# Performance work log

Measured on AMD Instinct MI355X. Metric: run time of the kernel, lower is better.

Reference implementation:

```python
import jax, jax.numpy as jnp
import numpy as np

B = 2097152  # batch of poses

def setup_inputs() -> dict:
    key = jax.random.key(0)
    ks = jax.random.split(key, 7)
    x = jax.random.normal(ks[0], (B, 7), dtype=jnp.float32)
    # PyTorch Linear init: U(-1/sqrt(fan_in), 1/sqrt(fan_in)); weights stored [out, in]
    def linear_params(kw, kb, fan_in, fan_out):
        bound = 1.0 / np.sqrt(fan_in)
        W = jax.random.uniform(kw, (fan_out, fan_in), minval=-bound, maxval=bound, dtype=jnp.float32)
        b = jax.random.uniform(kb, (fan_out,), minval=-bound, maxval=bound, dtype=jnp.float32)
        return W, b
    W1, b1 = linear_params(ks[1], ks[2], 7, 64)
    W2, b2 = linear_params(ks[3], ks[4], 64, 64)
    W3, b3 = linear_params(ks[5], ks[6], 64, 7)
    return {"x": x, "W1": W1, "b1": b1, "W2": W2, "b2": b2, "W3": W3, "b3": b3}

def reference(x, W1, b1, W2, b2, W3, b3):
    h = jax.nn.relu(x @ W1.T + b1)
    h = jax.nn.relu(h @ W2.T + b2)
    out = h @ W3.T + b3  # [B, 7]
    pos = out[:, :3]
    quat = out[:, 3:]
    quat = quat / jnp.linalg.norm(quat, axis=1, keepdims=True)
    return jnp.concatenate([pos, quat], axis=1)
```

## Files before the change

kernel.cpp:

```cpp
#include <hip/hip_runtime.h>
#include <math.h>


typedef _Float16 half8  __attribute__((ext_vector_type(8)));
typedef __fp16   fp16x2 __attribute__((ext_vector_type(2)));
typedef float    floatx16 __attribute__((ext_vector_type(16)));
typedef unsigned int uint2v __attribute__((ext_vector_type(2)));

#define MFMA32(a, b, c) __builtin_amdgcn_mfma_f32_32x32x16_f16((a), (b), (c), 0, 0, 0)
#define LO_SCALE 2.44140625e-4f

union PairU { fp16x2 h; unsigned int u; };
union FragU { unsigned int w[4]; half8 h; };

static __device__ inline void split_pack2(float v0, float v1,
                                          unsigned int& hw, unsigned int& lw) {
    PairU hp, lp;
    hp.h = __builtin_amdgcn_cvt_pkrtz(v0, v1);
    float f0 = (float)hp.h[0], f1 = (float)hp.h[1];
    lp.h = __builtin_amdgcn_cvt_pkrtz((v0 - f0) * 4096.0f,
                                      (v1 - f1) * 4096.0f);
    hw = hp.u; lw = lp.u;
}

static __device__ inline void swap32(unsigned int a, unsigned int b,
                                     unsigned int& lo, unsigned int& hi) {
    uint2v r = __builtin_amdgcn_permlane32_swap(a, b, false, false);
    lo = r[0]; hi = r[1];
}

__global__ __launch_bounds__(256, 2) void pose_mlp_mfma_t(
    const float* __restrict__ x,
    const float* __restrict__ W1, const float* __restrict__ b1,
    const float* __restrict__ W2, const float* __restrict__ b2,
    const float* __restrict__ W3, const float* __restrict__ b3,
    float* __restrict__ out, int nrows)
{
    const int tid  = threadIdx.x;
    const int lane = tid & 63;
    const int wv   = tid >> 6;
    const int g    = lane >> 5;
    const int n5   = lane & 31;

    half8 w2h[2][4], w2l[2][4];
#pragma unroll
    for (int ct = 0; ct < 2; ++ct) {
        const float* wrow = W2 + (ct * 32 + n5) * 64;
#pragma unroll
        for (int kb = 0; kb < 4; ++kb) {
            FragU H, L;
#pragma unroll
            for (int m = 0; m < 4; ++m) {
                float a0 = wrow[kb * 16 + g * 8 + 2 * m];
                float a1 = wrow[kb * 16 + g * 8 + 2 * m + 1];
                split_pack2(a0, a1, H.w[m], L.w[m]);
            }
            w2h[ct][kb] = H.h; w2l[ct][kb] = L.h;
        }
    }
    const bool nv = (n5 < 7);
    half8 w3h[4], w3l[4];
#pragma unroll
    for (int kb = 0; kb < 4; ++kb) {
        FragU H, L;
#pragma unroll
        for (int m = 0; m < 4; ++m) {
            float a0 = nv ? W3[n5 * 64 + kb * 16 + g * 8 + 2 * m] : 0.0f;
            float a1 = nv ? W3[n5 * 64 + kb * 16 + g * 8 + 2 * m + 1] : 0.0f;
            split_pack2(a0, a1, H.w[m], L.w[m]);
        }
        w3h[kb] = H.h; w3l[kb] = L.h;
    }
    half8 w1h[2], w1l[2];
#pragma unroll
    for (int ct = 0; ct < 2; ++ct) {
        FragU H, L;
#pragma unroll
        for (int m = 0; m < 4; ++m) {
            int k0 = 2 * m, k1 = 2 * m + 1;
            float a0 = (g == 0) ? W1[(ct * 32 + n5) * 7 + k0] : 0.0f;
            float a1 = (g == 0) ? ((k1 < 7) ? W1[(ct * 32 + n5) * 7 + k1]
                                            : b1[ct * 32 + n5]) : 0.0f;
            split_pack2(a0, a1, H.w[m], L.w[m]);
        }
        w1h[ct] = H.h; w1l[ct] = L.h;
    }
    float b2t[2][16];
#pragma unroll
    for (int ct = 0; ct < 2; ++ct)
#pragma unroll
        for (int i = 0; i < 16; ++i)
            b2t[ct][i] = b2[ct * 32 + (i & 3) + 8 * (i >> 2) + 4 * g];
    float b3t[4];
#pragma unroll
    for (int i = 0; i < 4; ++i)
        b3t[i] = g ? ((i < 3) ? b3[4 + i] : 0.0f) : b3[i];

    const int ITERS = 16;
    const int blk0 = blockIdx.x * (ITERS * 128);

    float xv[7] = {0.f,0.f,0.f,0.f,0.f,0.f,0.f};
    {
        int r = blk0 + wv * 32 + n5;
        if (g == 0 && r < nrows) {
            const float* xr = x + (size_t)r * 7;
#pragma unroll
            for (int j = 0; j < 7; ++j) xv[j] = xr[j];
        }
    }

    for (int it = 0; it < ITERS; ++it) {
        const int r0 = blk0 + it * 128 + wv * 32;

        FragU xH, xL;
        {
            float p0 = g ? 0.f : xv[0], p1 = g ? 0.f : xv[1];
            float p2 = g ? 0.f : xv[2], p3 = g ? 0.f : xv[3];
            float p4 = g ? 0.f : xv[4], p5 = g ? 0.f : xv[5];
            float p6 = g ? 0.f : xv[6], p7 = g ? 0.f : 1.0f;
            split_pack2(p0, p1, xH.w[0], xL.w[0]);
            split_pack2(p2, p3, xH.w[1], xL.w[1]);
            split_pack2(p4, p5, xH.w[2], xL.w[2]);
            split_pack2(p6, p7, xH.w[3], xL.w[3]);
        }
        if (it < ITERS - 1) {
            int r = r0 + 128 + n5;
            if (g == 0 && r < nrows) {
                const float* xr = x + (size_t)r * 7;
#pragma unroll
                for (int j = 0; j < 7; ++j) xv[j] = xr[j];
            }
        }

        unsigned int ownH[2][8], ownL[2][8];
#pragma unroll
        for (int ct = 0; ct < 2; ++ct) {
            floatx16 ah, al;
#pragma unroll
            for (int i = 0; i < 16; ++i) { ah[i] = 0.0f; al[i] = 0.0f; }
            ah = MFMA32(w1h[ct], xH.h, ah);
            al = MFMA32(w1h[ct], xL.h, al);
            al = MFMA32(w1l[ct], xH.h, al);
#pragma unroll
            for (int m = 0; m < 8; ++m) {
                float v0 = fmaxf(fmaf(al[2*m],   LO_SCALE, ah[2*m]),   0.0f);
                float v1 = fmaxf(fmaf(al[2*m+1], LO_SCALE, ah[2*m+1]), 0.0f);
                split_pack2(v0, v1, ownH[ct][m], ownL[ct][m]);
            }
        }

        half8 aH[4], aL[4];
#pragma unroll
        for (int kb = 0; kb < 4; ++kb) {
            const int c = kb >> 1, sA = (kb & 1) * 4, sB = sA + 2;
            FragU H, L;
            swap32(ownH[c][sA],   ownH[c][sB],   H.w[0], H.w[2]);
            swap32(ownH[c][sA+1], ownH[c][sB+1], H.w[1], H.w[3]);
            swap32(ownL[c][sA],   ownL[c][sB],   L.w[0], L.w[2]);
            swap32(ownL[c][sA+1], ownL[c][sB+1], L.w[1], L.w[3]);
            aH[kb] = H.h; aL[kb] = L.h;
        }

#pragma unroll
        for (int ct = 0; ct < 2; ++ct) {
            floatx16 ch, cl;
#pragma unroll
            for (int i = 0; i < 16; ++i) { ch[i] = b2t[ct][i]; cl[i] = 0.0f; }
#pragma unroll
            for (int kb = 0; kb < 4; ++kb) {
                ch = MFMA32(w2h[ct][kb], aH[kb], ch);
                cl = MFMA32(w2h[ct][kb], aL[kb], cl);
                cl = MFMA32(w2l[ct][kb], aH[kb], cl);
            }
#pragma unroll
            for (int m = 0; m < 8; ++m) {
                float v0 = fmaxf(fmaf(cl[2*m],   LO_SCALE, ch[2*m]),   0.0f);
                float v1 = fmaxf(fmaf(cl[2*m+1], LO_SCALE, ch[2*m+1]), 0.0f);
                split_pack2(v0, v1, ownH[ct][m], ownL[ct][m]);
            }
        }

#pragma unroll
        for (int kb = 0; kb < 4; ++kb) {
            const int c = kb >> 1, sA = (kb & 1) * 4, sB = sA + 2;
            FragU H, L;
            swap32(ownH[c][sA],   ownH[c][sB],   H.w[0], H.w[2]);
            swap32(ownH[c][sA+1], ownH[c][sB+1], H.w[1], H.w[3]);
            swap32(ownL[c][sA],   ownL[c][sB],   L.w[0], L.w[2]);
            swap32(ownL[c][sA+1], ownL[c][sB+1], L.w[1], L.w[3]);
            aH[kb] = H.h; aL[kb] = L.h;
        }

        {
            floatx16 oh, ol;
#pragma unroll
            for (int i = 0; i < 16; ++i) { oh[i] = 0.0f; ol[i] = 0.0f; }
#pragma unroll
            for (int kb = 0; kb < 4; ++kb) {
                oh = MFMA32(w3h[kb], aH[kb], oh);
                ol = MFMA32(w3h[kb], aL[kb], ol);
                ol = MFMA32(w3l[kb], aH[kb], ol);
            }
            float c0 = fmaf(ol[0], LO_SCALE, oh[0]) + b3t[0];
            float c1 = fmaf(ol[1], LO_SCALE, oh[1]) + b3t[1];
            float c2 = fmaf(ol[2], LO_SCALE, oh[2]) + b3t[2];
            float c3 = fmaf(ol[3], LO_SCALE, oh[3]) + b3t[3];

            float p = g ? fmaf(c2, c2, fmaf(c1, c1, c0 * c0)) : c3 * c3;
            unsigned int plo, phi;
            swap32(__float_as_uint(p), __float_as_uint(p), plo, phi);
            float other = __uint_as_float(g ? plo : phi);
            float s = p + other;
            float rn = 1.0f / sqrtf(s);

            int r = r0 + n5;
            if (r < nrows) {
                float* orow = out + (size_t)r * 7;
                if (g == 0) {
                    orow[0] = c0; orow[1] = c1; orow[2] = c2; orow[3] = c3 * rn;
                } else {
                    orow[4] = c0 * rn; orow[5] = c1 * rn; orow[6] = c2 * rn;
                }
            }
        }
    }
}

extern "C" void kernel_launch(void* const* d_in, const int* in_sizes, int n_in,
                              void* d_out, int out_size, void* d_ws, size_t ws_size,
                              hipStream_t stream)
{
    const float* x  = (const float*)d_in[0];
    const float* W1 = (const float*)d_in[1];
    const float* b1 = (const float*)d_in[2];
    const float* W2 = (const float*)d_in[3];
    const float* b2 = (const float*)d_in[4];
    const float* W3 = (const float*)d_in[5];
    const float* b3 = (const float*)d_in[6];
    float* out = (float*)d_out;

    const int nrows = in_sizes[0] / 7;
    const int rows_per_block = 16 * 128;
    const int grid = (nrows + rows_per_block - 1) / rows_per_block;
    pose_mlp_mfma_t<<<grid, 256, 0, stream>>>(x, W1, b1, W2, b2, W3, b3, out, nrows);
}
```

Measured before the change: 100.7 us.

## Permute W2/W3 K-columns to remove permlane32 swaps between MFMA layers

```diff
diff --git a/kernel.cpp b/kernel.cpp
--- a/kernel.cpp
+++ b/kernel.cpp
@@ -23,13 +23,21 @@
     hw = hp.u; lw = lp.u;
 }
 
+static __device__ inline int sigma_inv(int k) {
+    int ci = k >> 5, r = k & 31;
+    int m  = 4 * ((r >> 4) & 1) + ((r >> 1) & 3);
+    int i  = 2 * m + (r & 1);
+    int gD = (r >> 3) & 1;
+    return 32 * ci + (i & 3) + 8 * (i >> 2) + 4 * gD;
+}
+
 static __device__ inline void swap32(unsigned int a, unsigned int b,
                                      unsigned int& lo, unsigned int& hi) {
     uint2v r = __builtin_amdgcn_permlane32_swap(a, b, false, false);
     lo = r[0]; hi = r[1];
 }
 
-__global__ __launch_bounds__(256, 2) void pose_mlp_mfma_t(
+__global__ __launch_bounds__(256, 2) void pose_mlp_mfma_s(
     const float* __restrict__ x,
     const float* __restrict__ W1, const float* __restrict__ b1,
     const float* __restrict__ W2, const float* __restrict__ b2,
@@ -51,8 +59,9 @@
             FragU H, L;
 #pragma unroll
             for (int m = 0; m < 4; ++m) {
-                float a0 = wrow[kb * 16 + g * 8 + 2 * m];
-                float a1 = wrow[kb * 16 + g * 8 + 2 * m + 1];
+                int k0 = kb * 16 + g * 8 + 2 * m;
+                float a0 = wrow[sigma_inv(k0)];
+                float a1 = wrow[sigma_inv(k0 + 1)];
                 split_pack2(a0, a1, H.w[m], L.w[m]);
             }
             w2h[ct][kb] = H.h; w2l[ct][kb] = L.h;
@@ -65,8 +74,9 @@
         FragU H, L;
 #pragma unroll
         for (int m = 0; m < 4; ++m) {
-            float a0 = nv ? W3[n5 * 64 + kb * 16 + g * 8 + 2 * m] : 0.0f;
-            float a1 = nv ? W3[n5 * 64 + kb * 16 + g * 8 + 2 * m + 1] : 0.0f;
+            int k0 = kb * 16 + g * 8 + 2 * m;
+            float a0 = nv ? W3[n5 * 64 + sigma_inv(k0)]     : 0.0f;
+            float a1 = nv ? W3[n5 * 64 + sigma_inv(k0 + 1)] : 0.0f;
             split_pack2(a0, a1, H.w[m], L.w[m]);
         }
         w3h[kb] = H.h; w3l[kb] = L.h;
@@ -85,16 +95,21 @@
         }
         w1h[ct] = H.h; w1l[ct] = L.h;
     }
-    float b2t[2][16];
+
+    floatx16 zero16;
+#pragma unroll
+    for (int i = 0; i < 16; ++i) zero16[i] = 0.0f;
+    floatx16 bias2v[2];
 #pragma unroll
     for (int ct = 0; ct < 2; ++ct)
 #pragma unroll
         for (int i = 0; i < 16; ++i)
-            b2t[ct][i] = b2[ct * 32 + (i & 3) + 8 * (i >> 2) + 4 * g];
+            bias2v[ct][i] = b2[ct * 32 + (i & 3) + 8 * (i >> 2) + 4 * g];
     float b3t[4];
 #pragma unroll
     for (int i = 0; i < 4; ++i)
         b3t[i] = g ? ((i < 3) ? b3[4 + i] : 0.0f) : b3[i];
+    const float x7 = (g == 0) ? 1.0f : 0.0f;
 
     const int ITERS = 16;
     const int blk0 = blockIdx.x * (ITERS * 128);
@@ -113,16 +128,11 @@
         const int r0 = blk0 + it * 128 + wv * 32;
 
         FragU xH, xL;
-        {
-            float p0 = g ? 0.f : xv[0], p1 = g ? 0.f : xv[1];
-            float p2 = g ? 0.f : xv[2], p3 = g ? 0.f : xv[3];
-            float p4 = g ? 0.f : xv[4], p5 = g ? 0.f : xv[5];
-            float p6 = g ? 0.f : xv[6], p7 = g ? 0.f : 1.0f;
-            split_pack2(p0, p1, xH.w[0], xL.w[0]);
-            split_pack2(p2, p3, xH.w[1], xL.w[1]);
-            split_pack2(p4, p5, xH.w[2], xL.w[2]);
-            split_pack2(p6, p7, xH.w[3], xL.w[3]);
-        }
+        split_pack2(xv[0], xv[1], xH.w[0], xL.w[0]);
+        split_pack2(xv[2], xv[3], xH.w[1], xL.w[1]);
+        split_pack2(xv[4], xv[5], xH.w[2], xL.w[2]);
+        split_pack2(xv[6], x7,    xH.w[3], xL.w[3]);
+
         if (it < ITERS - 1) {
             int r = r0 + 128 + n5;
             if (g == 0 && r < nrows) {
@@ -132,74 +142,51 @@
             }
         }
 
-        unsigned int ownH[2][8], ownL[2][8];
+        FragU AH[4], AL[4];
 #pragma unroll
         for (int ct = 0; ct < 2; ++ct) {
-            floatx16 ah, al;
-#pragma unroll
-            for (int i = 0; i < 16; ++i) { ah[i] = 0.0f; al[i] = 0.0f; }
-            ah = MFMA32(w1h[ct], xH.h, ah);
-            al = MFMA32(w1h[ct], xL.h, al);
+            floatx16 ah = MFMA32(w1h[ct], xH.h, zero16);
+            floatx16 al = MFMA32(w1h[ct], xL.h, zero16);
             al = MFMA32(w1l[ct], xH.h, al);
 #pragma unroll
             for (int m = 0; m < 8; ++m) {
                 float v0 = fmaxf(fmaf(al[2*m],   LO_SCALE, ah[2*m]),   0.0f);
                 float v1 = fmaxf(fmaf(al[2*m+1], LO_SCALE, ah[2*m+1]), 0.0f);
-                split_pack2(v0, v1, ownH[ct][m], ownL[ct][m]);
-            }
-        }
-
-        half8 aH[4], aL[4];
-#pragma unroll
-        for (int kb = 0; kb < 4; ++kb) {
-            const int c = kb >> 1, sA = (kb & 1) * 4, sB = sA + 2;
-            FragU H, L;
-            swap32(ownH[c][sA],   ownH[c][sB],   H.w[0], H.w[2]);
-            swap32(ownH[c][sA+1], ownH[c][sB+1], H.w[1], H.w[3]);
-            swap32(ownL[c][sA],   ownL[c][sB],   L.w[0], L.w[2]);
-            swap32(ownL[c][sA+1], ownL[c][sB+1], L.w[1], L.w[3]);
-            aH[kb] = H.h; aL[kb] = L.h;
-        }
-
+                const int kb = 2 * ct + (m >> 2), w = m & 3;
+                split_pack2(v0, v1, AH[kb].w[w], AL[kb].w[w]);
+            }
+        }
+
+        FragU BH[4], BL[4];
 #pragma unroll
         for (int ct = 0; ct < 2; ++ct) {
-            floatx16 ch, cl;
-#pragma unroll
-            for (int i = 0; i < 16; ++i) { ch[i] = b2t[ct][i]; cl[i] = 0.0f; }
-#pragma unroll
-            for (int kb = 0; kb < 4; ++kb) {
-                ch = MFMA32(w2h[ct][kb], aH[kb], ch);
-                cl = MFMA32(w2h[ct][kb], aL[kb], cl);
-                cl = MFMA32(w2l[ct][kb], aH[kb], cl);
+            floatx16 ch = MFMA32(w2h[ct][0], AH[0].h, bias2v[ct]);
+            floatx16 cl = MFMA32(w2h[ct][0], AL[0].h, zero16);
+            cl = MFMA32(w2l[ct][0], AH[0].h, cl);
+#pragma unroll
+            for (int kb = 1; kb < 4; ++kb) {
+                ch = MFMA32(w2h[ct][kb], AH[kb].h, ch);
+                cl = MFMA32(w2h[ct][kb], AL[kb].h, cl);
+                cl = MFMA32(w2l[ct][kb], AH[kb].h, cl);
             }
 #pragma unroll
             for (int m = 0; m < 8; ++m) {
                 float v0 = fmaxf(fmaf(cl[2*m],   LO_SCALE, ch[2*m]),   0.0f);
                 float v1 = fmaxf(fmaf(cl[2*m+1], LO_SCALE, ch[2*m+1]), 0.0f);
-                split_pack2(v0, v1, ownH[ct][m], ownL[ct][m]);
-            }
-        }
-
-#pragma unroll
-        for (int kb = 0; kb < 4; ++kb) {
-            const int c = kb >> 1, sA = (kb & 1) * 4, sB = sA + 2;
-            FragU H, L;
-            swap32(ownH[c][sA],   ownH[c][sB],   H.w[0], H.w[2]);
-            swap32(ownH[c][sA+1], ownH[c][sB+1], H.w[1], H.w[3]);
-            swap32(ownL[c][sA],   ownL[c][sB],   L.w[0], L.w[2]);
-            swap32(ownL[c][sA+1], ownL[c][sB+1], L.w[1], L.w[3]);
-            aH[kb] = H.h; aL[kb] = L.h;
+                const int kb = 2 * ct + (m >> 2), w = m & 3;
+                split_pack2(v0, v1, BH[kb].w[w], BL[kb].w[w]);
+            }
         }
 
         {
-            floatx16 oh, ol;
-#pragma unroll
-            for (int i = 0; i < 16; ++i) { oh[i] = 0.0f; ol[i] = 0.0f; }
-#pragma unroll
-            for (int kb = 0; kb < 4; ++kb) {
-                oh = MFMA32(w3h[kb], aH[kb], oh);
-                ol = MFMA32(w3h[kb], aL[kb], ol);
-                ol = MFMA32(w3l[kb], aH[kb], ol);
+            floatx16 oh = MFMA32(w3h[0], BH[0].h, zero16);
+            floatx16 ol = MFMA32(w3h[0], BL[0].h, zero16);
+            ol = MFMA32(w3l[0], BH[0].h, ol);
+#pragma unroll
+            for (int kb = 1; kb < 4; ++kb) {
+                oh = MFMA32(w3h[kb], BH[kb].h, oh);
+                ol = MFMA32(w3h[kb], BL[kb].h, ol);
+                ol = MFMA32(w3l[kb], BH[kb].h, ol);
             }
             float c0 = fmaf(ol[0], LO_SCALE, oh[0]) + b3t[0];
             float c1 = fmaf(ol[1], LO_SCALE, oh[1]) + b3t[1];
@@ -242,5 +229,5 @@
     const int nrows = in_sizes[0] / 7;
     const int rows_per_block = 16 * 128;
     const int grid = (nrows + rows_per_block - 1) / rows_per_block;
-    pose_mlp_mfma_t<<<grid, 256, 0, stream>>>(x, W1, b1, W2, b2, W3, b3, out, nrows);
-}
+    pose_mlp_mfma_s<<<grid, 256, 0, stream>>>(x, W1, b1, W2, b2, W3, b3, out, nrows);
+}
```

Measured after the change: 102.4 us. About the same (+1.6%).
